# Performance work log

Measured on AMD Instinct MI355X. Metric: run time of the kernel, lower is better.

## Reference

```python
import jax, jax.numpy as jnp
import numpy as np

B, L, D, H = 2, 2048, 1024, 16
HD = D // H  # 64


def rotate_half(x):
    x1, x2 = x[..., : x.shape[-1] // 2], x[..., x.shape[-1] // 2 :]
    return jnp.concatenate([-x2, x1], axis=-1)


def apply_rope(x, cos, sin):
    # x: (B, H, L, HD); cos/sin: (1, L, HD)
    c = cos[:, None, : x.shape[2], :]
    s = sin[:, None, : x.shape[2], :]
    return x * c + rotate_half(x) * s


def setup_inputs() -> dict:
    key = jax.random.key(0)
    ks = jax.random.split(key, 16)
    query = jax.random.normal(ks[0], (B, L, D), jnp.float32)
    k_in = jax.random.normal(ks[1], (B, L, D), jnp.float32)
    v_in = jax.random.normal(ks[2], (B, L, D), jnp.float32)
    key_padding_mask = jax.random.uniform(ks[3], (B, L)) < 0.2
    # genuine RoPE tables
    inv_freq = 1.0 / (10000.0 ** (jnp.arange(0, HD, 2, dtype=jnp.float32) / HD))
    ang = jnp.arange(L, dtype=jnp.float32)[:, None] * inv_freq[None, :]  # (L, HD/2)
    ang = jnp.concatenate([ang, ang], axis=-1)  # (L, HD)
    rope_cos = jnp.cos(ang)[None]  # (1, L, HD)
    rope_sin = jnp.sin(ang)[None]
    scale = 0.02
    Wq = jax.random.normal(ks[4], (D, D), jnp.float32) * scale
    bq = jnp.zeros((D,), jnp.float32)
    Wk = jax.random.normal(ks[5], (D, D), jnp.float32) * scale
    bk = jnp.zeros((D,), jnp.float32)
    Wv = jax.random.normal(ks[6], (D, D), jnp.float32) * scale
    bv = jnp.zeros((D,), jnp.float32)
    Wg = jax.random.normal(ks[7], (D, D), jnp.float32) * scale  # init zeros in torch; random for grad coverage
    bg = jnp.ones((D,), jnp.float32)
    Wo = jax.random.normal(ks[8], (D, D), jnp.float32) * scale
    bo = jnp.zeros((D,), jnp.float32)
    return dict(query=query, key=k_in, value=v_in, key_padding_mask=key_padding_mask,
                rope_cos=rope_cos, rope_sin=rope_sin,
                Wq=Wq, bq=bq, Wk=Wk, bk=bk, Wv=Wv, bv=bv,
                Wg=Wg, bg=bg, Wo=Wo, bo=bo)


def reference(query, key, value, key_padding_mask, rope_cos, rope_sin,
              Wq, bq, Wk, bk, Wv, bv, Wg, bg, Wo, bo):
    Bq, Lq, _ = query.shape
    Lk = key.shape[1]
    # torch Linear: x @ W.T + b
    Q = (query @ Wq.T + bq).reshape(Bq, Lq, H, HD).transpose(0, 2, 1, 3)
    K = (key @ Wk.T + bk).reshape(Bq, Lk, H, HD).transpose(0, 2, 1, 3)
    V = (value @ Wv.T + bv).reshape(Bq, Lk, H, HD).transpose(0, 2, 1, 3)
    K = apply_rope(K, rope_cos, rope_sin)
    Q = apply_rope(Q, rope_cos, rope_sin)
    scale = 1.0 / jnp.sqrt(jnp.asarray(HD, query.dtype))
    scores = jnp.einsum('bhqd,bhkd->bhqk', Q, K) * scale
    allow = ~key_padding_mask[:, None, None, :]  # (B,1,1,Lk): True = attend
    scores = jnp.where(allow, scores, -jnp.inf)
    attn = jax.nn.softmax(scores, axis=-1)
    out = jnp.einsum('bhqk,bhkd->bhqd', attn, V)
    out = jnp.nan_to_num(out, nan=0.0)
    out = out.transpose(0, 2, 1, 3).reshape(Bq, Lq, D)
    gate = jax.nn.sigmoid(query @ Wg.T + bg)
    out = out * gate
    out = out @ Wo.T + bo
    return out
```

## Files before the change

### kernel.cpp

```cpp
#include <hip/hip_runtime.h>
#include <hip/hip_bf16.h>
#include <cstdint>


constexpr int NB = 2, NL = 2048, ND = 1024, NH = 16, NHD = 64;
constexpr int NM = NB * NL;

typedef __bf16 bf16_t;
typedef __bf16 bf16x8 __attribute__((ext_vector_type(8)));
typedef __bf16 bf16x4 __attribute__((ext_vector_type(4)));
typedef float f32x4 __attribute__((ext_vector_type(4)));
typedef float f32x16 __attribute__((ext_vector_type(16)));
typedef unsigned int uint2v __attribute__((ext_vector_type(2)));

typedef const __attribute__((address_space(1))) void* gas_ptr;
typedef __attribute__((address_space(3))) void* las_ptr;

__device__ __forceinline__ void async_load16(const void* g, void* l) {
  __builtin_amdgcn_global_load_lds((gas_ptr)g, (las_ptr)l, 16, 0, 0);
}

__device__ __forceinline__ unsigned cvtpk_bf16(float lo, float hi) {
  unsigned r;
  asm("v_cvt_pk_bf16_f32 %0, %1, %2" : "=v"(r) : "v"(lo), "v"(hi));
  return r;
}

__device__ __forceinline__ void pl32_swap(unsigned& a, unsigned& b) {
#if __has_builtin(__builtin_amdgcn_permlane32_swap)
  uint2v r = __builtin_amdgcn_permlane32_swap(a, b, false, false);
  a = r.x; b = r.y;
#else
  asm volatile("v_permlane32_swap_b32 %0, %1" : "+v"(a), "+v"(b));
#endif
}

struct CvtArgs {
  const float* s[8];
  bf16_t* d[8];
};
__global__ __launch_bounds__(256) void cvt8_kernel(CvtArgs a) {
  int y = blockIdx.y;
  int n4 = (y < 3) ? (NM * ND / 4) : (ND * ND / 4);
  const float* src = a.s[y];
  bf16_t* dst = a.d[y];
  for (int i = blockIdx.x * 256 + threadIdx.x; i < n4; i += gridDim.x * 256) {
    float4 v = ((const float4*)src)[i];
    bf16x4 o;
    o[0] = (bf16_t)v.x; o[1] = (bf16_t)v.y; o[2] = (bf16_t)v.z; o[3] = (bf16_t)v.w;
    ((bf16x4*)dst)[i] = o;
  }
}

__global__ __launch_bounds__(512, 2) void gemm8_kernel(
    const bf16_t* __restrict__ Aq, const bf16_t* __restrict__ Ak, const bf16_t* __restrict__ Av,
    const bf16_t* __restrict__ W0, const bf16_t* __restrict__ W1,
    const bf16_t* __restrict__ W2, const bf16_t* __restrict__ W3,
    const float* __restrict__ b0, const float* __restrict__ b1,
    const float* __restrict__ b2, const float* __restrict__ b3,
    const float* __restrict__ ctab, const float* __restrict__ stab,
    bf16_t* __restrict__ Qr, bf16_t* __restrict__ Kr, bf16_t* __restrict__ Vt,
    bf16_t* __restrict__ Gb) {
  extern __shared__ __align__(16) bf16_t smem[];
  bf16_t* lA = smem;
  bf16_t* lB = smem + 32768;

  const int tid = threadIdx.x, lane = tid & 63, w = tid >> 6;
  const int wm = w >> 2, wn = w & 3;
  const int lr = lane & 15, lg = lane >> 4;

  const int lin = blockIdx.x;
  const int xcd = lin & 7, idx = lin >> 3;
  const int nt = xcd * 2 + (idx & 1);
  const int mt = idx >> 1;
  const int t = nt >> 2;
  const bf16_t* Asrc = (t == 1) ? Ak : (t == 2) ? Av : Aq;
  const bf16_t* Wsrc = (t == 0) ? W0 : (t == 1) ? W1 : (t == 2) ? W2 : W3;
  const int nbase = (nt & 3) * 256;

  const int srow = lane >> 3;
  const int gcol = ((lane & 7) ^ srow) * 8;

  auto stageA = [&](int buf, int hf, int kt) {
#pragma unroll
    for (int jj = 0; jj < 2; ++jj) {
      int slot = jj * 8 + w;
      int r = slot * 8 + srow;
      async_load16(Asrc + (size_t)(mt * 256 + hf * 128 + r) * ND + kt * 64 + gcol,
                   lA + (buf * 2 + hf) * 8192 + slot * 512);
    }
  };
  auto stageB = [&](int buf, int hf, int kt) {
#pragma unroll
    for (int jj = 0; jj < 2; ++jj) {
      int slot = jj * 8 + w;
      int r = slot * 8 + srow;
      async_load16(Wsrc + (size_t)(nbase + hf * 128 + r) * ND + kt * 64 + gcol,
                   lB + (buf * 2 + hf) * 8192 + slot * 512);
    }
  };

  f32x4 acc[8][4];
#pragma unroll
  for (int i = 0; i < 8; ++i)
#pragma unroll
    for (int j = 0; j < 4; ++j)
#pragma unroll
      for (int k = 0; k < 4; ++k) acc[i][j][k] = 0.f;

  stageA(0, 0, 0); stageA(0, 1, 0); stageB(0, 0, 0); stageB(0, 1, 0);
  stageB(1, 0, 1); stageB(1, 1, 1);
  asm volatile("s_waitcnt vmcnt(4)" ::: "memory");
  __builtin_amdgcn_s_barrier();

  const bf16_t* Ab[2] = { lA + wm * 8192, lA + (2 + wm) * 8192 };
  const bf16_t* Bb[2] = { lB + (wn >> 1) * 8192 + (wn & 1) * 4096,
                          lB + (2 + (wn >> 1)) * 8192 + (wn & 1) * 4096 };

  for (int j = 0; j < 8; ++j) {
#pragma unroll
    for (int hp = 0; hp < 2; ++hp) {
      const bf16_t* Ap = Ab[hp];
      const bf16_t* Bp = Bb[hp];
      bf16x8 bfr[4][2];
#pragma unroll
      for (int p = 0; p < 4; ++p) {
        bf16x8 af[2][2];
#pragma unroll
        for (int mi = 0; mi < 2; ++mi)
#pragma unroll
          for (int ks = 0; ks < 2; ++ks)
            af[mi][ks] = *(const bf16x8*)(Ap + ((p * 2 + mi) * 16 + lr) * 64 +
                                          ((ks * 4 + lg) ^ (lr & 7)) * 8);
        if (p == 0) {
#pragma unroll
          for (int nj = 0; nj < 4; ++nj)
#pragma unroll
            for (int ks = 0; ks < 2; ++ks)
              bfr[nj][ks] = *(const bf16x8*)(Bp + (nj * 16 + lr) * 64 +
                                             ((ks * 4 + lg) ^ (lr & 7)) * 8);
        }
        if (hp == 0) {
          if (p == 0) stageA(1, 0, 2 * j + 1);
          if (p == 1) { stageA(1, 1, 2 * j + 1); if (j < 7) stageB(0, 0, 2 * j + 2); }
          if (p == 2) { if (j < 7) stageB(0, 1, 2 * j + 2); }
        } else if (j < 7) {
          if (p == 0) stageA(0, 0, 2 * j + 2);
          if (p == 1) { stageA(0, 1, 2 * j + 2); stageB(1, 0, 2 * j + 3); }
          if (p == 2) stageB(1, 1, 2 * j + 3);
        }
        __builtin_amdgcn_s_barrier();
        __builtin_amdgcn_s_setprio(1);
#pragma unroll
        for (int mi = 0; mi < 2; ++mi)
#pragma unroll
          for (int nj = 0; nj < 4; ++nj)
#pragma unroll
            for (int ks = 0; ks < 2; ++ks)
              acc[p * 2 + mi][nj] = __builtin_amdgcn_mfma_f32_16x16x32_bf16(
                  af[mi][ks], bfr[nj][ks], acc[p * 2 + mi][nj], 0, 0, 0);
        __builtin_amdgcn_s_setprio(0);
        if (p == 3) {
          if (hp == 0) {
            if (j < 7) { asm volatile("s_waitcnt vmcnt(4)" ::: "memory"); }
            else       { asm volatile("s_waitcnt vmcnt(0)" ::: "memory"); }
          } else if (j < 7) {
            asm volatile("s_waitcnt vmcnt(4)" ::: "memory");
          }
        }
        __builtin_amdgcn_s_barrier();
      }
    }
  }

  const int fbase = nbase + wn * 64;
  const int h = fbase >> 6;
  if (t < 2) {
    bf16_t* dst = (t == 0) ? Qr : Kr;
    const float* bias = (t == 0) ? b0 : b1;
    const float qs = (t == 0) ? 0.18033688011112042f : 1.0f;
#pragma unroll
    for (int i = 0; i < 8; ++i)
#pragma unroll
      for (int rg = 0; rg < 4; ++rg) {
        int mm = mt * 256 + wm * 128 + i * 16 + lg * 4 + rg;
        int bb = mm >> 11, l = mm & (NL - 1);
        bf16_t* rowp = dst + ((bb * NH + h) * NL + l) * NHD;
        const float* crow = ctab + l * NHD;
        const float* srw = stab + l * NHD;
#pragma unroll
        for (int nj = 0; nj < 2; ++nj) {
          int dlo = nj * 16 + lr, dhi = dlo + 32;
          float xlo = acc[i][nj][rg] + bias[fbase + dlo];
          float xhi = acc[i][nj + 2][rg] + bias[fbase + dhi];
          float olo = (xlo * crow[dlo] - xhi * srw[dlo]) * qs;
          float ohi = (xhi * crow[dhi] + xlo * srw[dhi]) * qs;
          rowp[dlo] = (bf16_t)olo;
          rowp[dhi] = (bf16_t)ohi;
        }
      }
  } else if (t == 2) {
#pragma unroll
    for (int i = 0; i < 8; ++i) {
      int mmb = mt * 256 + wm * 128 + i * 16 + lg * 4;
      int bb = mmb >> 11, l0 = mmb & (NL - 1);
#pragma unroll
      for (int nj = 0; nj < 4; ++nj) {
        int d = nj * 16 + lr;
        float bias = b2[fbase + d];
        unsigned u01 = cvtpk_bf16(acc[i][nj][0] + bias, acc[i][nj][1] + bias);
        unsigned u23 = cvtpk_bf16(acc[i][nj][2] + bias, acc[i][nj][3] + bias);
        unsigned long long pk = (unsigned long long)u01 | ((unsigned long long)u23 << 32);
        *(unsigned long long*)(Vt + ((bb * NH + h) * NHD + d) * NL + l0) = pk;
      }
    }
  } else {
#pragma unroll
    for (int i = 0; i < 8; ++i)
#pragma unroll
      for (int rg = 0; rg < 4; ++rg) {
        int mm = mt * 256 + wm * 128 + i * 16 + lg * 4 + rg;
#pragma unroll
        for (int nj = 0; nj < 4; ++nj) {
          int f = fbase + nj * 16 + lr;
          Gb[mm * ND + f] = (bf16_t)(acc[i][nj][rg] + b3[f]);
        }
      }
  }
}

__global__ __launch_bounds__(256) void gemm_out_kernel(
    const bf16_t* __restrict__ A, const bf16_t* __restrict__ W,
    const float* __restrict__ bias0, float* __restrict__ Out) {
  __shared__ __align__(16) bf16_t lA[2][128 * 64];
  __shared__ __align__(16) bf16_t lB[2][128 * 64];
  const int tid = threadIdx.x, lane = tid & 63, w = tid >> 6;
  const int wm = w >> 1, wn = w & 1;
  const int lr = lane & 15, lg = lane >> 4;

  const int lin = blockIdx.x;
  const int ntile = lin & 7, mtile = lin >> 3;

  const bf16_t* Ablk = A + mtile * 128 * ND;
  const bf16_t* Wblk = W + ntile * 128 * ND;

  f32x4 acc[4][4];
#pragma unroll
  for (int i = 0; i < 4; ++i)
#pragma unroll
    for (int j = 0; j < 4; ++j)
#pragma unroll
      for (int k = 0; k < 4; ++k) acc[i][j][k] = 0.f;

  auto STAGE = [&](int b, int kb) {
#pragma unroll
    for (int p = 0; p < 4; ++p) {
      int q = w * 256 + p * 64 + lane;
      int r = q >> 3, c = q & 7;
      int cs = c ^ (r & 7);
      async_load16(Ablk + r * ND + kb * 64 + cs * 8, &lA[b][(w * 256 + p * 64) * 8]);
      async_load16(Wblk + r * ND + kb * 64 + cs * 8, &lB[b][(w * 256 + p * 64) * 8]);
    }
  };
  auto COMPUTE = [&](int b) {
    const bf16_t* pA = lA[b];
    const bf16_t* pB = lB[b];
#pragma unroll
    for (int ks = 0; ks < 2; ++ks) {
      bf16x8 af[4], bfr[4];
#pragma unroll
      for (int i = 0; i < 4; ++i) {
        int ra = wm * 64 + i * 16 + lr;
        int ca = (ks * 4 + lg) ^ (ra & 7);
        af[i] = *(const bf16x8*)(pA + ra * 64 + ca * 8);
        int rb = wn * 64 + i * 16 + lr;
        int cb = (ks * 4 + lg) ^ (rb & 7);
        bfr[i] = *(const bf16x8*)(pB + rb * 64 + cb * 8);
      }
#pragma unroll
      for (int i = 0; i < 4; ++i)
#pragma unroll
        for (int j = 0; j < 4; ++j)
          acc[i][j] = __builtin_amdgcn_mfma_f32_16x16x32_bf16(af[i], bfr[j], acc[i][j], 0, 0, 0);
    }
  };

  STAGE(0, 0);
  __syncthreads();
  int buf = 0;
  for (int kb = 0; kb < 15; ++kb) {
    STAGE(buf ^ 1, kb + 1);
    COMPUTE(buf);
    __syncthreads();
    buf ^= 1;
  }
  COMPUTE(buf);

#pragma unroll
  for (int j = 0; j < 4; ++j) {
    int nn = ntile * 128 + wn * 64 + j * 16 + lr;
    float bias = bias0[nn];
#pragma unroll
    for (int i = 0; i < 4; ++i)
#pragma unroll
      for (int rg = 0; rg < 4; ++rg) {
        int mm = mtile * 128 + wm * 64 + i * 16 + lg * 4 + rg;
        Out[mm * ND + nn] = acc[i][j][rg] + bias;
      }
  }
}

__global__ __launch_bounds__(256) void attn_kernel(
    const bf16_t* __restrict__ Qr, const bf16_t* __restrict__ Kr, const bf16_t* __restrict__ Vt,
    const int* __restrict__ mask, const bf16_t* __restrict__ Gb, bf16_t* __restrict__ X) {
  __shared__ __align__(16) bf16_t lK[2][128 * 64];
  __shared__ __align__(16) bf16_t lV[2][64 * 128];

  int lin = blockIdx.y * gridDim.x + blockIdx.x;
  int swz = (lin & 7) * 64 + (lin >> 3);
  const int qb = swz & 15, bh = swz >> 4;
  const int bb = bh >> 4, h = bh & 15;

  const int tid = threadIdx.x, lane = tid & 63, w = tid >> 6;
  const int ql = lane & 31, hi = lane >> 5;

  const bf16_t* Kbh = Kr + bh * NL * NHD;
  const bf16_t* Vbh = Vt + bh * NHD * NL;
  const int q = qb * 128 + w * 32 + ql;

  const bf16_t* Qp = Qr + (bh * NL + q) * NHD + 8 * hi;
  bf16x8 qf[4];
#pragma unroll
  for (int c = 0; c < 4; ++c) qf[c] = *(const bf16x8*)(Qp + 16 * c);
  bf16x8 qf5 = {};
  qf5[0] = (bf16_t)(hi ? 0.f : 1.f);

  f32x16 acc[2];
#pragma unroll
  for (int dt = 0; dt < 2; ++dt)
#pragma unroll
    for (int r = 0; r < 16; ++r) acc[dt][r] = 0.f;
  float lrun = 0.f;

  const bf16_t* gsrc[8];
#pragma unroll
  for (int j = 0; j < 8; ++j) {
    if (j < 4) {
      int u = j * 256 + tid;
      int r = u >> 3, c = u & 7, cs = c ^ (r & 7);
      gsrc[j] = Kbh + r * NHD + cs * 8;
    } else {
      int v = (j - 4) * 256 + tid;
      int r = v >> 4, c = v & 15, cs = (c & 8) | ((c & 7) ^ (r & 7));
      gsrc[j] = Vbh + r * NL + cs * 8;
    }
  }
  auto STAGE = [&](int b) {
#pragma unroll
    for (int j = 0; j < 8; ++j) {
      if (j < 4) {
        async_load16(gsrc[j], &lK[b][(j * 256 + tid) * 8]);
        gsrc[j] += 128 * NHD;
      } else {
        async_load16(gsrc[j], &lV[b][((j - 4) * 256 + tid) * 8]);
        gsrc[j] += 128;
      }
    }
  };

  unsigned rdK[2][4], rdV[2][4];
#pragma unroll
  for (int t2 = 0; t2 < 2; ++t2)
#pragma unroll
    for (int c = 0; c < 4; ++c) {
      unsigned un = ((2 * c + hi) ^ (ql & 7)) * 16;
      rdK[t2][c] = (32 * t2 + ql) * 128 + un;
      rdV[t2][c] = (32 * t2 + ql) * 256 + un;
    }
  const char* lKc = (const char*)lK;
  const char* lVc = (const char*)lV;

  STAGE(0);
  int mv0 = mask[bb * NL + lane];
  int mv1 = mask[bb * NL + 64 + lane];
  __syncthreads();

  auto BODY = [&](int buf, int t) {
    int nmv0 = 0, nmv1 = 0;
    if (t < 15) {
      STAGE(buf ^ 1);
      nmv0 = mask[bb * NL + (t + 1) * 128 + lane];
      nmv1 = mask[bb * NL + (t + 1) * 128 + 64 + lane];
    }
    unsigned long long bmA = __ballot(mv0 != 0);
    unsigned long long bmB = __ballot(mv1 != 0);
    unsigned mws[4] = {(unsigned)bmA, (unsigned)(bmA >> 32),
                       (unsigned)bmB, (unsigned)(bmB >> 32)};
    bf16x8 kf5[4];
#pragma unroll
    for (int g = 0; g < 4; ++g) {
      float bv = ((mws[g] >> ql) & 1u) ? -1008.f : -8.f;
      bf16x8 z = {};
      z[0] = (bf16_t)(hi ? 0.f : bv);
      kf5[g] = z;
    }
    float ts[16];
#pragma unroll
    for (int hh = 0; hh < 2; ++hh) {
      f32x16 st[2];
      __builtin_amdgcn_s_setprio(1);
#pragma unroll
      for (int t2 = 0; t2 < 2; ++t2) {
        f32x16 s;
#pragma unroll
        for (int r = 0; r < 16; ++r) s[r] = 0.f;
#pragma unroll
        for (int c = 0; c < 4; ++c) {
          bf16x8 kf = *(const bf16x8*)(lKc + rdK[t2][c] + buf * 16384 + hh * 8192);
          s = __builtin_amdgcn_mfma_f32_32x32x16_bf16(kf, qf[c], s, 0, 0, 0);
        }
        s = __builtin_amdgcn_mfma_f32_32x32x16_bf16(kf5[hh * 2 + t2], qf5, s, 0, 0, 0);
        st[t2] = s;
      }
      __builtin_amdgcn_s_setprio(0);

#pragma unroll
      for (int t2 = 0; t2 < 2; ++t2)
#pragma unroll
        for (int r = 0; r < 16; ++r) st[t2][r] = exp2f(st[t2][r]);
#pragma unroll
      for (int r = 0; r < 16; ++r) {
        float v = st[0][r] + st[1][r];
        if (hh == 0) ts[r] = v; else ts[r] += v;
      }

      unsigned wds[2][4][2];
#pragma unroll
      for (int t2 = 0; t2 < 2; ++t2)
#pragma unroll
        for (int r1 = 0; r1 < 4; ++r1) {
          wds[t2][r1][0] = cvtpk_bf16(st[t2][4 * r1 + 0], st[t2][4 * r1 + 1]);
          wds[t2][r1][1] = cvtpk_bf16(st[t2][4 * r1 + 2], st[t2][4 * r1 + 3]);
        }
      bf16x8 pf[4];
#pragma unroll
      for (int kc = 0; kc < 4; ++kc) {
        int t2 = kc >> 1, r1a = 2 * (kc & 1);
        unsigned a0 = wds[t2][r1a][0], b0 = wds[t2][r1a + 1][0];
        unsigned a1 = wds[t2][r1a][1], b1 = wds[t2][r1a + 1][1];
        pl32_swap(a0, b0);
        pl32_swap(a1, b1);
        union { unsigned u[4]; bf16x8 v; } uu;
        uu.u[0] = a0; uu.u[1] = a1; uu.u[2] = b0; uu.u[3] = b1;
        pf[kc] = uu.v;
      }

      __builtin_amdgcn_s_setprio(1);
#pragma unroll
      for (int dt = 0; dt < 2; ++dt) {
        f32x16 a = acc[dt];
#pragma unroll
        for (int kc = 0; kc < 4; ++kc) {
          bf16x8 vf = *(const bf16x8*)(lVc + rdV[dt][kc] + buf * 16384 + hh * 128);
          a = __builtin_amdgcn_mfma_f32_32x32x16_bf16(vf, pf[kc], a, 0, 0, 0);
        }
        acc[dt] = a;
      }
      __builtin_amdgcn_s_setprio(0);
    }
#pragma unroll
    for (int off = 8; off > 0; off >>= 1)
#pragma unroll
      for (int r = 0; r < 8; ++r)
        if (r < off) ts[r] += ts[r + off];
    lrun += ts[0];
    __syncthreads();
    mv0 = nmv0;
    mv1 = nmv1;
  };

  for (int tt = 0; tt < 8; ++tt) {
    BODY(0, 2 * tt);
    BODY(1, 2 * tt + 1);
  }

  float lt = lrun + __shfl_xor(lrun, 32, 64);
  float rinv = lt > 0.f ? 1.f / lt : 0.f;
  const int rowbase = (bb * NL + q) * ND + h * NHD;
#pragma unroll
  for (int dt = 0; dt < 2; ++dt)
#pragma unroll
    for (int r1 = 0; r1 < 4; ++r1) {
      int dbase = 32 * dt + 8 * r1 + 4 * hi;
      bf16x4 g4 = *(const bf16x4*)(Gb + rowbase + dbase);
      bf16x4 o;
#pragma unroll
      for (int j = 0; j < 4; ++j) {
        float gate = 1.f / (1.f + exp2f(-1.44269504f * (float)g4[j]));
        o[j] = (bf16_t)(acc[dt][4 * r1 + j] * rinv * gate);
      }
      *(bf16x4*)(X + rowbase + dbase) = o;
    }
}

extern "C" void kernel_launch(void* const* d_in, const int* in_sizes, int n_in,
                              void* d_out, int out_size, void* d_ws, size_t ws_size,
                              hipStream_t stream) {
  const float* query = (const float*)d_in[0];
  const float* key   = (const float*)d_in[1];
  const float* value = (const float*)d_in[2];
  const int*   maskp = (const int*)d_in[3];
  const float* rcos  = (const float*)d_in[4];
  const float* rsin  = (const float*)d_in[5];
  const float* Wq = (const float*)d_in[6];  const float* bq = (const float*)d_in[7];
  const float* Wk = (const float*)d_in[8];  const float* bk = (const float*)d_in[9];
  const float* Wv = (const float*)d_in[10]; const float* bv = (const float*)d_in[11];
  const float* Wg = (const float*)d_in[12]; const float* bg = (const float*)d_in[13];
  const float* Wo = (const float*)d_in[14]; const float* bo = (const float*)d_in[15];

  constexpr size_t MB = 1ull << 20;
  char* ws = (char*)d_ws;
  bf16_t* qbb = (bf16_t*)(ws + 0 * MB);
  bf16_t* kbb = (bf16_t*)(ws + 8 * MB);
  bf16_t* vbb = (bf16_t*)(ws + 16 * MB);
  bf16_t* wqb = (bf16_t*)(ws + 24 * MB);
  bf16_t* wkb = (bf16_t*)(ws + 26 * MB);
  bf16_t* wvb = (bf16_t*)(ws + 28 * MB);
  bf16_t* wgb = (bf16_t*)(ws + 30 * MB);
  bf16_t* wob = (bf16_t*)(ws + 32 * MB);
  bf16_t* Qr  = (bf16_t*)(ws + 34 * MB);
  bf16_t* Kr  = (bf16_t*)(ws + 42 * MB);
  bf16_t* Vt  = (bf16_t*)(ws + 50 * MB);
  bf16_t* Gb  = (bf16_t*)(ws + 58 * MB);
  bf16_t* Xb  = (bf16_t*)(ws + 74 * MB);

  CvtArgs ca;
  ca.s[0] = query; ca.d[0] = qbb;
  ca.s[1] = key;   ca.d[1] = kbb;
  ca.s[2] = value; ca.d[2] = vbb;
  ca.s[3] = Wq;    ca.d[3] = wqb;
  ca.s[4] = Wk;    ca.d[4] = wkb;
  ca.s[5] = Wv;    ca.d[5] = wvb;
  ca.s[6] = Wg;    ca.d[6] = wgb;
  ca.s[7] = Wo;    ca.d[7] = wob;
  cvt8_kernel<<<dim3(1024, 8), 256, 0, stream>>>(ca);

  gemm8_kernel<<<256, 512, 131072, stream>>>(
      qbb, kbb, vbb, wqb, wkb, wvb, wgb, bq, bk, bv, bg, rcos, rsin,
      Qr, Kr, Vt, Gb);

  attn_kernel<<<dim3(16, 32), 256, 0, stream>>>(Qr, Kr, Vt, maskp, Gb, Xb);

  gemm_out_kernel<<<256, 256, 0, stream>>>(Xb, wob, bo, (float*)d_out);
}
```

Baseline: 145.3 us.

## Rework attention kernel to 16x16 MFMA tiles with eight waves per block

Rewrites the attention inner loop to use 16x16 MFMA instructions. Each of eight waves now owns 16 queries, so blocks grow to 512 threads. The score layout now feeds the P·V MFMA directly, which removes the permlane32 swap shuffles. The extra bias MFMA that applied the key-padding mask is replaced by a per-element select after exp2, and row sums are reduced through shuffles plus a small shared array. The trade-off is more LDS fragment reads per MFMA and scalar, less vectorized output stores, in exchange for simpler register layout and more waves to hide latency.

```diff
diff --git a/kernel.cpp b/kernel.cpp
--- a/kernel.cpp
+++ b/kernel.cpp
@@ -9,8 +9,8 @@
 typedef __bf16 bf16_t;
 typedef __bf16 bf16x8 __attribute__((ext_vector_type(8)));
 typedef __bf16 bf16x4 __attribute__((ext_vector_type(4)));
+typedef short s16x4 __attribute__((ext_vector_type(4)));
 typedef float f32x4 __attribute__((ext_vector_type(4)));
-typedef float f32x16 __attribute__((ext_vector_type(16)));
 typedef unsigned int uint2v __attribute__((ext_vector_type(2)));
 
 typedef const __attribute__((address_space(1))) void* gas_ptr;
@@ -26,12 +26,12 @@
   return r;
 }
 
-__device__ __forceinline__ void pl32_swap(unsigned& a, unsigned& b) {
-#if __has_builtin(__builtin_amdgcn_permlane32_swap)
-  uint2v r = __builtin_amdgcn_permlane32_swap(a, b, false, false);
-  a = r.x; b = r.y;
+__device__ __forceinline__ f32x4 mfma16x16x16(s16x4 a, s16x4 b, f32x4 c) {
+#if __has_builtin(__builtin_amdgcn_mfma_f32_16x16x16bf16_1k)
+  return __builtin_amdgcn_mfma_f32_16x16x16bf16_1k(a, b, c, 0, 0, 0);
 #else
-  asm volatile("v_permlane32_swap_b32 %0, %1" : "+v"(a), "+v"(b));
+  asm volatile("v_mfma_f32_16x16x16_bf16 %0, %1, %2, %0" : "+v"(c) : "v"(a), "v"(b));
+  return c;
 #endif
 }
 
@@ -310,11 +310,12 @@
   }
 }
 
-__global__ __launch_bounds__(256) void attn_kernel(
+__global__ __launch_bounds__(512, 4) void attn_kernel(
     const bf16_t* __restrict__ Qr, const bf16_t* __restrict__ Kr, const bf16_t* __restrict__ Vt,
     const int* __restrict__ mask, const bf16_t* __restrict__ Gb, bf16_t* __restrict__ X) {
   __shared__ __align__(16) bf16_t lK[2][128 * 64];
   __shared__ __align__(16) bf16_t lV[2][64 * 128];
+  __shared__ float lSm[8][16];
 
   int lin = blockIdx.y * gridDim.x + blockIdx.x;
   int swz = (lin & 7) * 64 + (lin >> 3);
@@ -322,60 +323,60 @@
   const int bb = bh >> 4, h = bh & 15;
 
   const int tid = threadIdx.x, lane = tid & 63, w = tid >> 6;
-  const int ql = lane & 31, hi = lane >> 5;
+  const int lr = lane & 15, lg = lane >> 4;
 
   const bf16_t* Kbh = Kr + bh * NL * NHD;
   const bf16_t* Vbh = Vt + bh * NHD * NL;
-  const int q = qb * 128 + w * 32 + ql;
-
-  const bf16_t* Qp = Qr + (bh * NL + q) * NHD + 8 * hi;
-  bf16x8 qf[4];
-#pragma unroll
-  for (int c = 0; c < 4; ++c) qf[c] = *(const bf16x8*)(Qp + 16 * c);
-  bf16x8 qf5 = {};
-  qf5[0] = (bf16_t)(hi ? 0.f : 1.f);
-
-  f32x16 acc[2];
-#pragma unroll
-  for (int dt = 0; dt < 2; ++dt)
-#pragma unroll
-    for (int r = 0; r < 16; ++r) acc[dt][r] = 0.f;
-  float lrun = 0.f;
-
-  const bf16_t* gsrc[8];
-#pragma unroll
-  for (int j = 0; j < 8; ++j) {
-    if (j < 4) {
-      int u = j * 256 + tid;
+  const int q0 = qb * 128 + w * 16;
+
+  const bf16_t* Qp = Qr + (bh * NL + q0 + lr) * NHD + lg * 8;
+  bf16x8 qf[2];
+  qf[0] = *(const bf16x8*)(Qp);
+  qf[1] = *(const bf16x8*)(Qp + 32);
+
+  f32x4 acc[4];
+#pragma unroll
+  for (int dt = 0; dt < 4; ++dt)
+#pragma unroll
+    for (int k = 0; k < 4; ++k) acc[dt][k] = 0.f;
+  f32x4 lacc = {0.f, 0.f, 0.f, 0.f};
+
+  const bf16_t* gsrc[4];
+#pragma unroll
+  for (int j = 0; j < 4; ++j) {
+    if (j < 2) {
+      int u = j * 512 + tid;
       int r = u >> 3, c = u & 7, cs = c ^ (r & 7);
       gsrc[j] = Kbh + r * NHD + cs * 8;
     } else {
-      int v = (j - 4) * 256 + tid;
+      int v = (j - 2) * 512 + tid;
       int r = v >> 4, c = v & 15, cs = (c & 8) | ((c & 7) ^ (r & 7));
       gsrc[j] = Vbh + r * NL + cs * 8;
     }
   }
   auto STAGE = [&](int b) {
 #pragma unroll
-    for (int j = 0; j < 8; ++j) {
-      if (j < 4) {
-        async_load16(gsrc[j], &lK[b][(j * 256 + tid) * 8]);
+    for (int j = 0; j < 4; ++j) {
+      if (j < 2) {
+        async_load16(gsrc[j], &lK[b][(j * 512 + tid) * 8]);
         gsrc[j] += 128 * NHD;
       } else {
-        async_load16(gsrc[j], &lV[b][((j - 4) * 256 + tid) * 8]);
+        async_load16(gsrc[j], &lV[b][((j - 2) * 512 + tid) * 8]);
         gsrc[j] += 128;
       }
     }
   };
 
-  unsigned rdK[2][4], rdV[2][4];
-#pragma unroll
-  for (int t2 = 0; t2 < 2; ++t2)
-#pragma unroll
-    for (int c = 0; c < 4; ++c) {
-      unsigned un = ((2 * c + hi) ^ (ql & 7)) * 16;
-      rdK[t2][c] = (32 * t2 + ql) * 128 + un;
-      rdV[t2][c] = (32 * t2 + ql) * 256 + un;
+  unsigned kgr[2], vgo[2][4];
+#pragma unroll
+  for (int ks = 0; ks < 2; ++ks) kgr[ks] = (((ks * 4 + lg) ^ (lr & 7)) * 16);
+#pragma unroll
+  for (int hh = 0; hh < 2; ++hh)
+#pragma unroll
+    for (int T = 0; T < 4; ++T) {
+      unsigned g = hh * 8 + T * 2 + (lg >> 1);
+      unsigned gs = (g & 8) | ((g & 7) ^ (lr & 7));
+      vgo[hh][T] = gs * 16 + (lg & 1) * 8;
     }
   const char* lKc = (const char*)lK;
   const char* lVc = (const char*)lV;
@@ -394,86 +395,52 @@
     }
     unsigned long long bmA = __ballot(mv0 != 0);
     unsigned long long bmB = __ballot(mv1 != 0);
-    unsigned mws[4] = {(unsigned)bmA, (unsigned)(bmA >> 32),
-                       (unsigned)bmB, (unsigned)(bmB >> 32)};
-    bf16x8 kf5[4];
-#pragma unroll
-    for (int g = 0; g < 4; ++g) {
-      float bv = ((mws[g] >> ql) & 1u) ? -1008.f : -8.f;
-      bf16x8 z = {};
-      z[0] = (bf16_t)(hi ? 0.f : bv);
-      kf5[g] = z;
-    }
-    float ts[16];
 #pragma unroll
     for (int hh = 0; hh < 2; ++hh) {
-      f32x16 st[2];
+      unsigned long long bm = hh ? bmB : bmA;
+      f32x4 st[4];
       __builtin_amdgcn_s_setprio(1);
 #pragma unroll
-      for (int t2 = 0; t2 < 2; ++t2) {
-        f32x16 s;
-#pragma unroll
-        for (int r = 0; r < 16; ++r) s[r] = 0.f;
-#pragma unroll
-        for (int c = 0; c < 4; ++c) {
-          bf16x8 kf = *(const bf16x8*)(lKc + rdK[t2][c] + buf * 16384 + hh * 8192);
-          s = __builtin_amdgcn_mfma_f32_32x32x16_bf16(kf, qf[c], s, 0, 0, 0);
-        }
-        s = __builtin_amdgcn_mfma_f32_32x32x16_bf16(kf5[hh * 2 + t2], qf5, s, 0, 0, 0);
-        st[t2] = s;
+      for (int T = 0; T < 4; ++T) {
+        f32x4 s = {-8.f, -8.f, -8.f, -8.f};
+#pragma unroll
+        for (int ks = 0; ks < 2; ++ks) {
+          bf16x8 kf = *(const bf16x8*)(lKc + buf * 16384 +
+                                       (hh * 64 + T * 16 + lr) * 128 + kgr[ks]);
+          s = __builtin_amdgcn_mfma_f32_16x16x32_bf16(kf, qf[ks], s, 0, 0, 0);
+        }
+        st[T] = s;
       }
       __builtin_amdgcn_s_setprio(0);
-
-#pragma unroll
-      for (int t2 = 0; t2 < 2; ++t2)
-#pragma unroll
-        for (int r = 0; r < 16; ++r) st[t2][r] = exp2f(st[t2][r]);
-#pragma unroll
-      for (int r = 0; r < 16; ++r) {
-        float v = st[0][r] + st[1][r];
-        if (hh == 0) ts[r] = v; else ts[r] += v;
-      }
-
-      unsigned wds[2][4][2];
-#pragma unroll
-      for (int t2 = 0; t2 < 2; ++t2)
-#pragma unroll
-        for (int r1 = 0; r1 < 4; ++r1) {
-          wds[t2][r1][0] = cvtpk_bf16(st[t2][4 * r1 + 0], st[t2][4 * r1 + 1]);
-          wds[t2][r1][1] = cvtpk_bf16(st[t2][4 * r1 + 2], st[t2][4 * r1 + 3]);
-        }
-      bf16x8 pf[4];
-#pragma unroll
-      for (int kc = 0; kc < 4; ++kc) {
-        int t2 = kc >> 1, r1a = 2 * (kc & 1);
-        unsigned a0 = wds[t2][r1a][0], b0 = wds[t2][r1a + 1][0];
-        unsigned a1 = wds[t2][r1a][1], b1 = wds[t2][r1a + 1][1];
-        pl32_swap(a0, b0);
-        pl32_swap(a1, b1);
-        union { unsigned u[4]; bf16x8 v; } uu;
-        uu.u[0] = a0; uu.u[1] = a1; uu.u[2] = b0; uu.u[3] = b1;
-        pf[kc] = uu.v;
-      }
-
+      unsigned pk[4][2];
+#pragma unroll
+      for (int T = 0; T < 4; ++T) {
+        unsigned nib = (unsigned)(bm >> (T * 16 + lg * 4)) & 0xFu;
+        f32x4 p;
+#pragma unroll
+        for (int rg = 0; rg < 4; ++rg) {
+          float e = exp2f(st[T][rg]);
+          p[rg] = ((nib >> rg) & 1u) ? 0.f : e;
+        }
+        lacc += p;
+        pk[T][0] = cvtpk_bf16(p[0], p[1]);
+        pk[T][1] = cvtpk_bf16(p[2], p[3]);
+      }
       __builtin_amdgcn_s_setprio(1);
 #pragma unroll
-      for (int dt = 0; dt < 2; ++dt) {
-        f32x16 a = acc[dt];
-#pragma unroll
-        for (int kc = 0; kc < 4; ++kc) {
-          bf16x8 vf = *(const bf16x8*)(lVc + rdV[dt][kc] + buf * 16384 + hh * 128);
-          a = __builtin_amdgcn_mfma_f32_32x32x16_bf16(vf, pf[kc], a, 0, 0, 0);
+      for (int dt = 0; dt < 4; ++dt) {
+        f32x4 a = acc[dt];
+#pragma unroll
+        for (int T = 0; T < 4; ++T) {
+          s16x4 vb = *(const s16x4*)(lVc + buf * 16384 + (dt * 16 + lr) * 256 + vgo[hh][T]);
+          union { unsigned u[2]; s16x4 v; } ap;
+          ap.u[0] = pk[T][0]; ap.u[1] = pk[T][1];
+          a = mfma16x16x16(ap.v, vb, a);
         }
         acc[dt] = a;
       }
       __builtin_amdgcn_s_setprio(0);
     }
-#pragma unroll
-    for (int off = 8; off > 0; off >>= 1)
-#pragma unroll
-      for (int r = 0; r < 8; ++r)
-        if (r < off) ts[r] += ts[r + off];
-    lrun += ts[0];
     __syncthreads();
     mv0 = nmv0;
     mv1 = nmv1;
@@ -484,23 +451,24 @@
     BODY(1, 2 * tt + 1);
   }
 
-  float lt = lrun + __shfl_xor(lrun, 32, 64);
-  float rinv = lt > 0.f ? 1.f / lt : 0.f;
-  const int rowbase = (bb * NL + q) * ND + h * NHD;
-#pragma unroll
-  for (int dt = 0; dt < 2; ++dt)
-#pragma unroll
-    for (int r1 = 0; r1 < 4; ++r1) {
-      int dbase = 32 * dt + 8 * r1 + 4 * hi;
-      bf16x4 g4 = *(const bf16x4*)(Gb + rowbase + dbase);
-      bf16x4 o;
-#pragma unroll
-      for (int j = 0; j < 4; ++j) {
-        float gate = 1.f / (1.f + exp2f(-1.44269504f * (float)g4[j]));
-        o[j] = (bf16_t)(acc[dt][4 * r1 + j] * rinv * gate);
-      }
-      *(bf16x4*)(X + rowbase + dbase) = o;
-    }
+  float lt = lacc[0] + lacc[1] + lacc[2] + lacc[3];
+  lt += __shfl_xor(lt, 16, 64);
+  lt += __shfl_xor(lt, 32, 64);
+  if (lg == 0) lSm[w][lr] = (lt > 0.f) ? 1.f / lt : 0.f;
+  __syncthreads();
+
+#pragma unroll
+  for (int rg = 0; rg < 4; ++rg) {
+    float rinv = lSm[w][4 * lg + rg];
+    int row = bb * NL + q0 + 4 * lg + rg;
+#pragma unroll
+    for (int dt = 0; dt < 4; ++dt) {
+      int col = h * NHD + dt * 16 + lr;
+      float g = (float)Gb[row * ND + col];
+      float gate = 1.f / (1.f + exp2f(-1.44269504f * g));
+      X[row * ND + col] = (bf16_t)(acc[dt][rg] * rinv * gate);
+    }
+  }
 }
 
 extern "C" void kernel_launch(void* const* d_in, const int* in_sizes, int n_in,
@@ -549,7 +517,7 @@
       qbb, kbb, vbb, wqb, wkb, wvb, wgb, bq, bk, bv, bg, rcos, rsin,
       Qr, Kr, Vt, Gb);
 
-  attn_kernel<<<dim3(16, 32), 256, 0, stream>>>(Qr, Kr, Vt, maskp, Gb, Xb);
+  attn_kernel<<<dim3(16, 32), 512, 0, stream>>>(Qr, Kr, Vt, maskp, Gb, Xb);
 
   gemm_out_kernel<<<256, 256, 0, stream>>>(Xb, wob, bo, (float*)d_out);
 }
```

New measurement: 151.6 us. 1.04x slower.
